# Kernel tuning notes

Hardware: AMD Instinct MI355X
Metric: run time of the kernel (lower is better)

The kernel has to match this reference:

```python
import jax, jax.numpy as jnp
import numpy as np

LATENT = 256


def setup_inputs() -> dict:
    key = jax.random.key(0)
    ks = jax.random.split(key, 10)
    B, T, V, E, D0, H, L = 512, 200, 3356, 1128, 20000, 1024, LATENT

    def glorot(k, shape):
        fan_out, fan_in = shape
        std = np.sqrt(2.0 / (fan_in + fan_out)).astype(np.float32)
        return jax.random.normal(k, shape, dtype=jnp.float32) * std

    x = jax.random.uniform(ks[0], (B, D0), dtype=jnp.float32)
    item_ids = jax.random.randint(ks[1], (B, T), 0, V, dtype=jnp.int32)
    embed = jax.random.normal(ks[2], (V, E), dtype=jnp.float32)
    Wi = glorot(ks[3], (L, E))
    bi = jnp.zeros((L,), jnp.float32)
    We1 = glorot(ks[4], (H, D0))
    be1 = jnp.zeros((H,), jnp.float32)
    We2 = glorot(ks[5], (2 * L, H))
    be2 = jnp.zeros((2 * L,), jnp.float32)
    Wd1 = glorot(ks[6], (H, L))
    bd1 = jnp.zeros((H,), jnp.float32)
    Wd2 = glorot(ks[7], (D0, H))
    bd2 = jnp.zeros((D0,), jnp.float32)
    # dropout(p=0.5) mask, pre-scaled by 1/(1-p)=2
    drop_mask = (jax.random.bernoulli(ks[8], 0.5, (B, D0))).astype(jnp.float32) * 2.0
    eps = jax.random.normal(ks[9], (B, L), dtype=jnp.float32)
    return {"x": x, "item_ids": item_ids, "embed": embed, "Wi": Wi, "bi": bi,
            "We1": We1, "be1": be1, "We2": We2, "be2": be2,
            "Wd1": Wd1, "bd1": bd1, "Wd2": Wd2, "bd2": bd2,
            "drop_mask": drop_mask, "eps": eps}


def reference(x, item_ids, embed, Wi, bi, We1, be1, We2, be2,
              Wd1, bd1, Wd2, bd2, drop_mask, eps):
    # item feature path: embedding lookup -> linear -> per-sequence stats
    item = jnp.einsum('bte,le->btl', embed[item_ids], Wi) + bi        # [B,T,L]
    mean = jnp.mean(item, axis=1)                                      # [B,L]
    deviation = jnp.std(item, axis=1, ddof=1)                          # torch.std (unbiased)

    # encoder: F.normalize (L2 over features) -> dropout -> tanh MLP
    xn = x / jnp.maximum(jnp.linalg.norm(x, axis=1, keepdims=True), 1e-12)
    h = xn * drop_mask
    h = jnp.tanh(h @ We1.T + be1)
    gparams = h @ We2.T + be2                                          # [B,2L]
    mu, logvar = gparams[:, :LATENT], gparams[:, LATENT:]

    # reparam: MVN with diagonal covariance diag(deviation) == mean + sqrt(dev)*eps
    prior = mean + jnp.sqrt(deviation) * eps
    z = prior * jnp.exp(0.5 * logvar) + mu

    # decoder: tanh MLP
    hd = jnp.tanh(z @ Wd1.T + bd1)
    recon_x = hd @ Wd2.T + bd2                                         # [B,D0]
    return recon_x, mu, logvar
```

## Files before the change

### kernel.cpp

```cpp
#include <hip/hip_runtime.h>
#include <hip/hip_bf16.h>

typedef __bf16 bf16x8 __attribute__((ext_vector_type(8)));
typedef float f32x4 __attribute__((ext_vector_type(4)));
typedef unsigned short u16x8 __attribute__((ext_vector_type(8)));

static __device__ __forceinline__ unsigned short f2bf(float f){
  unsigned int u = __float_as_uint(f);
  u += 0x7fffu + ((u >> 16) & 1u);
  return (unsigned short)(u >> 16);
}

static __device__ __forceinline__ u16x8 cvt8(const float4& a, const float4& b){
  u16x8 r;
  r[0]=f2bf(a.x); r[1]=f2bf(a.y); r[2]=f2bf(a.z); r[3]=f2bf(a.w);
  r[4]=f2bf(b.x); r[5]=f2bf(b.y); r[6]=f2bf(b.z); r[7]=f2bf(b.w);
  return r;
}

static __device__ __forceinline__ void gload16(const void* g, void* l){
  __builtin_amdgcn_global_load_lds(
      (const __attribute__((address_space(1))) unsigned int*)g,
      (__attribute__((address_space(3))) unsigned int*)l, 16, 0, 0);
}

static __device__ __forceinline__ int xcd_remap(int o, int nwg){
  const int NX = 8;
  int q = nwg / NX, r = nwg % NX;
  int xcd = o % NX, pos = o / NX;
  return (xcd < r ? xcd * (q + 1) : r * (q + 1) + (xcd - r) * q) + pos;
}

template<int EPI>
__global__ __launch_bounds__(256) void gemm_bf(
    const unsigned short* __restrict__ A, const unsigned short* __restrict__ Bw,
    const float* __restrict__ bias,
    float* __restrict__ Cf, unsigned short* __restrict__ Cbf,
    int M, int N, int K, int kchunk)
{
  constexpr int BM = 128, BN = 128, BK = 32, BUF = (BM + BN) * BK;
  __shared__ unsigned short lds[3 * BUF];

  const int gx = gridDim.x, gy = gridDim.y;
  const int nwg = gx * gy * gridDim.z;
  int o = blockIdx.x + gx * (blockIdx.y + gy * blockIdx.z);
  int v = xcd_remap(o, nwg);
  const int bx = v % gx; v /= gx;
  const int by = v % gy; const int bz = v / gy;

  const int tid  = threadIdx.x, lane = tid & 63, wave = tid >> 6;
  const int bm0  = by * BM, bn0 = bx * BN;
  const int k0   = bz * kchunk;
  const int kend = min(K, k0 + kchunk);
  const int fr = lane & 15, fq = lane >> 4;
  const int wm = (wave >> 1) * 64, wn = (wave & 1) * 64;

  const bool isA  = wave < 2;
  const int cbase = (wave & 1) * 4;
  const int srow  = lane >> 2, scol = (lane & 3) * 8;
  const unsigned short* G = isA ? A : Bw;
  const int glim = (isA ? M : N) - 1;
  const int g0   = isA ? bm0 : bn0;
  const int loff = isA ? 0 : BM * BK;

  const int nk = (kend - k0) / BK;

  auto stage = [&](int buf, int t){
    unsigned short* dst = lds + buf * BUF + loff;
    const int kk = k0 + t * BK;
    #pragma unroll
    for (int c = 0; c < 4; c++) {
      const int ch = cbase + c;
      const int r = min(g0 + ch * 16 + srow, glim);
      gload16(G + (size_t)r * K + kk + scol, (char*)dst + ch * 1024);
    }
  };

  if (nk > 0) stage(0, 0);
  if (nk > 1) stage(1, 1);
  if (nk > 2) stage(2, 2);

  f32x4 acc[4][4] = {};
  int cur = 0;

  for (int t = 0; t < nk; ++t) {
    const int rem = nk - t - 1;
    if (rem >= 2)      asm volatile("s_waitcnt vmcnt(8)" ::: "memory");
    else if (rem == 1) asm volatile("s_waitcnt vmcnt(4)" ::: "memory");
    else               asm volatile("s_waitcnt vmcnt(0)" ::: "memory");
    __builtin_amdgcn_s_barrier();
    __builtin_amdgcn_sched_barrier(0);

    const unsigned short* lA = lds + cur * BUF;
    const unsigned short* lB = lA + BM * BK;
    u16x8 af[4], bg[4];
    #pragma unroll
    for (int i = 0; i < 4; i++) af[i] = *(const u16x8*)&lA[(wm + i*16 + fr) * BK + fq * 8];
    #pragma unroll
    for (int j = 0; j < 4; j++) bg[j] = *(const u16x8*)&lB[(wn + j*16 + fr) * BK + fq * 8];

    #pragma unroll
    for (int i = 0; i < 4; i++)
      #pragma unroll
      for (int j = 0; j < 4; j++)
        acc[i][j] = __builtin_amdgcn_mfma_f32_16x16x32_bf16(
            __builtin_bit_cast(bf16x8, af[i]),
            __builtin_bit_cast(bf16x8, bg[j]),
            acc[i][j], 0, 0, 0);

    asm volatile("s_waitcnt lgkmcnt(0)" ::: "memory");
    __builtin_amdgcn_sched_barrier(0);
    __builtin_amdgcn_s_barrier();
    if (t + 3 < nk) stage(cur, t + 3);
    cur = (cur == 2) ? 0 : cur + 1;
  }

  #pragma unroll
  for (int i = 0; i < 4; i++)
    #pragma unroll
    for (int j = 0; j < 4; j++)
      #pragma unroll
      for (int r = 0; r < 4; r++) {
        int row = bm0 + wm + i*16 + fq*4 + r;
        int col = bn0 + wn + j*16 + fr;
        if (row < M && col < N) {
          float v2 = acc[i][j][r];
          if constexpr (EPI == 0) {
            Cf[(size_t)row * N + col] = v2 + (bias ? bias[col] : 0.0f);
          } else if constexpr (EPI == 1) {
            atomicAdd(&Cf[(size_t)row * N + col], v2);
          } else {
            Cbf[(size_t)row * N + col] = f2bf(tanhf(v2 + bias[col]));
          }
        }
      }
}

__global__ __launch_bounds__(256) void cvt4_kernel(
    const float* __restrict__ s0, unsigned short* __restrict__ d0, int n0,
    const float* __restrict__ s1, unsigned short* __restrict__ d1, int n1,
    const float* __restrict__ s2, unsigned short* __restrict__ d2, int n2,
    const float* __restrict__ s3, unsigned short* __restrict__ d3, int n3,
    int nunits16)
{
  const int stride = gridDim.x * 256;
  for (int u = blockIdx.x * 256 + threadIdx.x; u < nunits16; u += stride) {
    int i = u * 16;
    const float* s; unsigned short* d;
    if (i < n0)              { s = s0; d = d0; }
    else if ((i -= n0) < n1) { s = s1; d = d1; }
    else if ((i -= n1) < n2) { s = s2; d = d2; }
    else                     { i -= n2; s = s3; d = d3; }
    const float4* q = (const float4*)(s + i);
    float4 a0 = q[0], a1 = q[1], a2 = q[2], a3 = q[3];
    *(u16x8*)(d + i)     = cvt8(a0, a1);
    *(u16x8*)(d + i + 8) = cvt8(a2, a3);
  }
}

__global__ __launch_bounds__(256) void cvtpad_kernel(
    const float* __restrict__ src, unsigned short* __restrict__ dst,
    int rows, int scols, int dcols)
{
  int i8 = blockIdx.x * 256 + threadIdx.x;
  int c8 = dcols / 8;
  if (i8 >= rows * c8) return;
  int r = i8 / c8, c0 = (i8 % c8) * 8;
  const float* s = src + (size_t)r * scols;
  u16x8 o;
  #pragma unroll
  for (int e = 0; e < 8; e++) { int c = c0 + e; o[e] = (c < scols) ? f2bf(s[c]) : (unsigned short)0; }
  *(u16x8*)(dst + (size_t)r * dcols + c0) = o;
}

__global__ __launch_bounds__(256) void ynorm_kernel(
    const float* __restrict__ x, const float* __restrict__ dm,
    unsigned short* __restrict__ y, float* __restrict__ ninv, int D0)
{
  const int b = blockIdx.x, tid = threadIdx.x;
  const float4* x4 = (const float4*)(x + (size_t)b * D0);
  const float4* d4 = (const float4*)(dm + (size_t)b * D0);
  ushort4* y4 = (ushort4*)(y + (size_t)b * D0);
  const int n4 = D0 / 4;
  float ss = 0.f;
  for (int i = tid; i < n4; i += 256) {
    float4 xv = x4[i], dv = d4[i];
    ss += xv.x*xv.x + xv.y*xv.y + xv.z*xv.z + xv.w*xv.w;
    ushort4 o;
    o.x = f2bf(xv.x*dv.x); o.y = f2bf(xv.y*dv.y);
    o.z = f2bf(xv.z*dv.z); o.w = f2bf(xv.w*dv.w);
    y4[i] = o;
  }
  #pragma unroll
  for (int off = 32; off > 0; off >>= 1) ss += __shfl_down(ss, off);
  __shared__ float wsum[4];
  if ((tid & 63) == 0) wsum[tid >> 6] = ss;
  __syncthreads();
  if (tid == 0) {
    float t = wsum[0] + wsum[1] + wsum[2] + wsum[3];
    ninv[b] = 1.0f / fmaxf(sqrtf(t), 1e-12f);
  }
}

__global__ __launch_bounds__(256) void stats_kernel(
    const float* __restrict__ proj, const int* __restrict__ ids,
    const float* __restrict__ bi, const float* __restrict__ eps,
    float* __restrict__ prior, int T)
{
  const int b = blockIdx.x, l = threadIdx.x;
  __shared__ int sid[256];
  if (l < T) sid[l] = ids[b * T + l];
  __syncthreads();
  float s1 = 0.f, s2 = 0.f;
  #pragma unroll 4
  for (int t = 0; t < T; t++) {
    float p = proj[(size_t)sid[t] * 256 + l];
    s1 += p; s2 += p * p;
  }
  float var = fmaxf((s2 - s1 * s1 / (float)T) / (float)(T - 1), 0.f);
  float dev = sqrtf(var);
  float mean = s1 / (float)T + bi[l];
  prior[b * 256 + l] = mean + sqrtf(dev) * eps[b * 256 + l];
}

__global__ __launch_bounds__(256) void epi1_kernel(
    const float* __restrict__ C1, const float* __restrict__ ninv,
    const float* __restrict__ be1, unsigned short* __restrict__ h)
{
  int i = blockIdx.x * 256 + threadIdx.x;
  int b = i >> 10, n = i & 1023;
  h[i] = f2bf(tanhf(ninv[b] * C1[i] + be1[n]));
}

__global__ __launch_bounds__(256) void z_kernel(
    const float* __restrict__ gp, const float* __restrict__ prior,
    const float* __restrict__ be2,
    float* __restrict__ out_mu, float* __restrict__ out_lv,
    unsigned short* __restrict__ z)
{
  int i = blockIdx.x * 256 + threadIdx.x;
  int b = i >> 8, l = i & 255;
  float mu = gp[b * 512 + l]       + be2[l];
  float lv = gp[b * 512 + 256 + l] + be2[256 + l];
  out_mu[i] = mu;
  out_lv[i] = lv;
  z[i] = f2bf(prior[i] * expf(0.5f * lv) + mu);
}

extern "C" void kernel_launch(void* const* d_in, const int* in_sizes, int n_in,
                              void* d_out, int out_size, void* d_ws, size_t ws_size,
                              hipStream_t stream)
{
  const float* x     = (const float*)d_in[0];
  const int*   ids   = (const int*)  d_in[1];
  const float* embed = (const float*)d_in[2];
  const float* Wi    = (const float*)d_in[3];
  const float* bi    = (const float*)d_in[4];
  const float* We1   = (const float*)d_in[5];
  const float* be1   = (const float*)d_in[6];
  const float* We2   = (const float*)d_in[7];
  const float* be2   = (const float*)d_in[8];
  const float* Wd1   = (const float*)d_in[9];
  const float* bd1   = (const float*)d_in[10];
  const float* Wd2   = (const float*)d_in[11];
  const float* bd2   = (const float*)d_in[12];
  const float* dm    = (const float*)d_in[13];
  const float* eps   = (const float*)d_in[14];

  constexpr int B = 512, T = 200, V = 3356, E = 1128, Ep = 1152, D0 = 20000, H = 1024, L = 256;

  char* w = (char*)d_ws;
  auto carve = [&](size_t bytes) { char* p = w; w += (bytes + 255) & ~(size_t)255; return p; };
  unsigned short* We1b  = (unsigned short*)carve((size_t)H * D0 * 2);
  unsigned short* Wd2b  = (unsigned short*)carve((size_t)D0 * H * 2);
  unsigned short* We2b  = (unsigned short*)carve((size_t)2 * L * H * 2);
  unsigned short* Wd1b  = (unsigned short*)carve((size_t)H * L * 2);
  unsigned short* embedb= (unsigned short*)carve((size_t)V * Ep * 2);
  unsigned short* Wib   = (unsigned short*)carve((size_t)L * Ep * 2);
  float*          proj  = (float*)         carve((size_t)V * L * 4);
  unsigned short* y     = (unsigned short*)carve((size_t)B * D0 * 2);
  float*          C1    = (float*)         carve((size_t)B * H * 4);
  unsigned short* h     = (unsigned short*)carve((size_t)B * H * 2);
  float*          gp    = (float*)         carve((size_t)B * 2 * L * 4);
  float*          prior = (float*)         carve((size_t)B * L * 4);
  unsigned short* z     = (unsigned short*)carve((size_t)B * L * 2);
  unsigned short* hd    = (unsigned short*)carve((size_t)B * H * 2);
  float*          ninv  = (float*)         carve((size_t)B * 4);

  float* out_recon = (float*)d_out;
  float* out_mu    = out_recon + (size_t)B * D0;
  float* out_lv    = out_mu + (size_t)B * L;

  {
    const int n0 = H * D0, n1 = D0 * H, n2 = 2 * L * H, n3 = H * L;
    const int nunits16 = (n0 + n1 + n2 + n3) / 16;
    cvt4_kernel<<<2048, 256, 0, stream>>>(We1, We1b, n0, Wd2, Wd2b, n1,
                                          We2, We2b, n2, Wd1, Wd1b, n3, nunits16);
  }
  cvtpad_kernel<<<(V * (Ep/8) + 255) / 256, 256, 0, stream>>>(embed, embedb, V, E, Ep);
  cvtpad_kernel<<<(L * (Ep/8) + 255) / 256, 256, 0, stream>>>(Wi, Wib, L, E, Ep);

  ynorm_kernel<<<B, 256, 0, stream>>>(x, dm, y, ninv, D0);

  hipMemsetAsync(proj, 0, (size_t)V * L * 4, stream);
  gemm_bf<1><<<dim3(2, 27, 4), 256, 0, stream>>>(
      embedb, Wib, nullptr, proj, nullptr, V, L, Ep, 288);
  stats_kernel<<<B, 256, 0, stream>>>(proj, ids, bi, eps, prior, T);

  hipMemsetAsync(C1, 0, (size_t)B * H * 4, stream);
  gemm_bf<1><<<dim3(8, 4, 25), 256, 0, stream>>>(
      y, We1b, nullptr, C1, nullptr, B, H, D0, 800);
  epi1_kernel<<<(B * H) / 256, 256, 0, stream>>>(C1, ninv, be1, h);

  hipMemsetAsync(gp, 0, (size_t)B * 2 * L * 4, stream);
  gemm_bf<1><<<dim3(4, 4, 4), 256, 0, stream>>>(
      h, We2b, nullptr, gp, nullptr, B, 2 * L, H, 256);
  z_kernel<<<(B * L) / 256, 256, 0, stream>>>(gp, prior, be2, out_mu, out_lv, z);

  gemm_bf<2><<<dim3(8, 4, 1), 256, 0, stream>>>(
      z, Wd1b, bd1, nullptr, hd, B, H, L, 256);
  gemm_bf<0><<<dim3(157, 4, 1), 256, 0, stream>>>(
      hd, Wd2b, bd2, out_recon, nullptr, B, D0, H, 1024);
}
```

Baseline: 277.4 us.

## Single-barrier GEMM pipeline with prefetch distance two; merge prep kernels into one launch

The GEMM main loop drops its second barrier per K-step. The next stage load is now issued right after the top barrier into the buffer two ahead, so prefetch depth falls from three tiles to two. Separately, the weight conversion, embedding/Wi padding conversion and x-normalization kernels are merged into one block-indexed prep kernel to cut launch overhead and let those jobs run side by side. The shallower prefetch may expose more memory latency, and sizes are now hardcoded as constexpr in the prep kernel.

```diff
diff --git a/kernel.cpp b/kernel.cpp
--- a/kernel.cpp
+++ b/kernel.cpp
@@ -78,18 +78,20 @@
 
   if (nk > 0) stage(0, 0);
   if (nk > 1) stage(1, 1);
-  if (nk > 2) stage(2, 2);
 
   f32x4 acc[4][4] = {};
   int cur = 0;
 
   for (int t = 0; t < nk; ++t) {
-    const int rem = nk - t - 1;
-    if (rem >= 2)      asm volatile("s_waitcnt vmcnt(8)" ::: "memory");
-    else if (rem == 1) asm volatile("s_waitcnt vmcnt(4)" ::: "memory");
-    else               asm volatile("s_waitcnt vmcnt(0)" ::: "memory");
+    if (t < nk - 1) asm volatile("s_waitcnt vmcnt(4)" ::: "memory");
+    else            asm volatile("s_waitcnt vmcnt(0)" ::: "memory");
     __builtin_amdgcn_s_barrier();
     __builtin_amdgcn_sched_barrier(0);
+
+    if (t + 2 < nk) {
+      int sb = cur + 2; if (sb >= 3) sb -= 3;
+      stage(sb, t + 2);
+    }
 
     const unsigned short* lA = lds + cur * BUF;
     const unsigned short* lB = lA + BM * BK;
@@ -107,11 +109,6 @@
             __builtin_bit_cast(bf16x8, af[i]),
             __builtin_bit_cast(bf16x8, bg[j]),
             acc[i][j], 0, 0, 0);
-
-    asm volatile("s_waitcnt lgkmcnt(0)" ::: "memory");
-    __builtin_amdgcn_sched_barrier(0);
-    __builtin_amdgcn_s_barrier();
-    if (t + 3 < nk) stage(cur, t + 3);
     cur = (cur == 2) ? 0 : cur + 1;
   }
 
@@ -136,33 +133,10 @@
       }
 }
 
-__global__ __launch_bounds__(256) void cvt4_kernel(
-    const float* __restrict__ s0, unsigned short* __restrict__ d0, int n0,
-    const float* __restrict__ s1, unsigned short* __restrict__ d1, int n1,
-    const float* __restrict__ s2, unsigned short* __restrict__ d2, int n2,
-    const float* __restrict__ s3, unsigned short* __restrict__ d3, int n3,
-    int nunits16)
-{
-  const int stride = gridDim.x * 256;
-  for (int u = blockIdx.x * 256 + threadIdx.x; u < nunits16; u += stride) {
-    int i = u * 16;
-    const float* s; unsigned short* d;
-    if (i < n0)              { s = s0; d = d0; }
-    else if ((i -= n0) < n1) { s = s1; d = d1; }
-    else if ((i -= n1) < n2) { s = s2; d = d2; }
-    else                     { i -= n2; s = s3; d = d3; }
-    const float4* q = (const float4*)(s + i);
-    float4 a0 = q[0], a1 = q[1], a2 = q[2], a3 = q[3];
-    *(u16x8*)(d + i)     = cvt8(a0, a1);
-    *(u16x8*)(d + i + 8) = cvt8(a2, a3);
-  }
-}
-
-__global__ __launch_bounds__(256) void cvtpad_kernel(
+static __device__ __forceinline__ void cvtpad_body(
     const float* __restrict__ src, unsigned short* __restrict__ dst,
-    int rows, int scols, int dcols)
-{
-  int i8 = blockIdx.x * 256 + threadIdx.x;
+    int rows, int scols, int dcols, int i8)
+{
   int c8 = dcols / 8;
   if (i8 >= rows * c8) return;
   int r = i8 / c8, c0 = (i8 % c8) * 8;
@@ -173,32 +147,65 @@
   *(u16x8*)(dst + (size_t)r * dcols + c0) = o;
 }
 
-__global__ __launch_bounds__(256) void ynorm_kernel(
+__global__ __launch_bounds__(256) void prep_kernel(
+    const float* __restrict__ We1, unsigned short* __restrict__ We1b,
+    const float* __restrict__ Wd2, unsigned short* __restrict__ Wd2b,
+    const float* __restrict__ We2, unsigned short* __restrict__ We2b,
+    const float* __restrict__ Wd1, unsigned short* __restrict__ Wd1b,
+    const float* __restrict__ embed, unsigned short* __restrict__ embedb,
+    const float* __restrict__ Wi, unsigned short* __restrict__ Wib,
     const float* __restrict__ x, const float* __restrict__ dm,
-    unsigned short* __restrict__ y, float* __restrict__ ninv, int D0)
-{
-  const int b = blockIdx.x, tid = threadIdx.x;
-  const float4* x4 = (const float4*)(x + (size_t)b * D0);
-  const float4* d4 = (const float4*)(dm + (size_t)b * D0);
-  ushort4* y4 = (ushort4*)(y + (size_t)b * D0);
-  const int n4 = D0 / 4;
-  float ss = 0.f;
-  for (int i = tid; i < n4; i += 256) {
-    float4 xv = x4[i], dv = d4[i];
-    ss += xv.x*xv.x + xv.y*xv.y + xv.z*xv.z + xv.w*xv.w;
-    ushort4 o;
-    o.x = f2bf(xv.x*dv.x); o.y = f2bf(xv.y*dv.y);
-    o.z = f2bf(xv.z*dv.z); o.w = f2bf(xv.w*dv.w);
-    y4[i] = o;
-  }
-  #pragma unroll
-  for (int off = 32; off > 0; off >>= 1) ss += __shfl_down(ss, off);
-  __shared__ float wsum[4];
-  if ((tid & 63) == 0) wsum[tid >> 6] = ss;
-  __syncthreads();
-  if (tid == 0) {
-    float t = wsum[0] + wsum[1] + wsum[2] + wsum[3];
-    ninv[b] = 1.0f / fmaxf(sqrtf(t), 1e-12f);
+    unsigned short* __restrict__ y, float* __restrict__ ninv)
+{
+  constexpr int D0 = 20000, H = 1024, L = 256, V = 3356, E = 1128, Ep = 1152;
+  constexpr int n0 = H * D0, n1 = D0 * H, n2 = 2 * L * H, n3 = H * L;
+  constexpr int CVT_B = 2048, YN_B = 512;
+  constexpr int PE_B = (V * (Ep / 8) + 255) / 256;
+  const int bb = blockIdx.x, tid = threadIdx.x;
+
+  if (bb < CVT_B) {
+    constexpr int nunits16 = (n0 + n1 + n2 + n3) / 16;
+    const int stride = CVT_B * 256;
+    for (int u = bb * 256 + tid; u < nunits16; u += stride) {
+      int i = u * 16;
+      const float* s; unsigned short* d;
+      if (i < n0)              { s = We1; d = We1b; }
+      else if ((i -= n0) < n1) { s = Wd2; d = Wd2b; }
+      else if ((i -= n1) < n2) { s = We2; d = We2b; }
+      else                     { i -= n2; s = Wd1; d = Wd1b; }
+      const float4* q = (const float4*)(s + i);
+      float4 a0 = q[0], a1 = q[1], a2 = q[2], a3 = q[3];
+      *(u16x8*)(d + i)     = cvt8(a0, a1);
+      *(u16x8*)(d + i + 8) = cvt8(a2, a3);
+    }
+  } else if (bb < CVT_B + YN_B) {
+    const int b = bb - CVT_B;
+    const float4* x4 = (const float4*)(x + (size_t)b * D0);
+    const float4* d4 = (const float4*)(dm + (size_t)b * D0);
+    ushort4* y4 = (ushort4*)(y + (size_t)b * D0);
+    const int n4 = D0 / 4;
+    float ss = 0.f;
+    for (int i = tid; i < n4; i += 256) {
+      float4 xv = x4[i], dv = d4[i];
+      ss += xv.x*xv.x + xv.y*xv.y + xv.z*xv.z + xv.w*xv.w;
+      ushort4 ov;
+      ov.x = f2bf(xv.x*dv.x); ov.y = f2bf(xv.y*dv.y);
+      ov.z = f2bf(xv.z*dv.z); ov.w = f2bf(xv.w*dv.w);
+      y4[i] = ov;
+    }
+    #pragma unroll
+    for (int off = 32; off > 0; off >>= 1) ss += __shfl_down(ss, off);
+    __shared__ float wsum[4];
+    if ((tid & 63) == 0) wsum[tid >> 6] = ss;
+    __syncthreads();
+    if (tid == 0) {
+      float t = wsum[0] + wsum[1] + wsum[2] + wsum[3];
+      ninv[b] = 1.0f / fmaxf(sqrtf(t), 1e-12f);
+    }
+  } else if (bb < CVT_B + YN_B + PE_B) {
+    cvtpad_body(embed, embedb, V, E, Ep, (bb - (CVT_B + YN_B)) * 256 + tid);
+  } else {
+    cvtpad_body(Wi, Wib, L, E, Ep, (bb - (CVT_B + YN_B + PE_B)) * 256 + tid);
   }
 }
 
@@ -292,15 +299,13 @@
   float* out_lv    = out_mu + (size_t)B * L;
 
   {
-    const int n0 = H * D0, n1 = D0 * H, n2 = 2 * L * H, n3 = H * L;
-    const int nunits16 = (n0 + n1 + n2 + n3) / 16;
-    cvt4_kernel<<<2048, 256, 0, stream>>>(We1, We1b, n0, Wd2, Wd2b, n1,
-                                          We2, We2b, n2, Wd1, Wd1b, n3, nunits16);
+    constexpr int CVT_B = 2048, YN_B = 512;
+    constexpr int PE_B = (V * (Ep / 8) + 255) / 256;
+    constexpr int PW_B = (L * (Ep / 8) + 255) / 256;
+    prep_kernel<<<CVT_B + YN_B + PE_B + PW_B, 256, 0, stream>>>(
+        We1, We1b, Wd2, Wd2b, We2, We2b, Wd1, Wd1b,
+        embed, embedb, Wi, Wib, x, dm, y, ninv);
   }
-  cvtpad_kernel<<<(V * (Ep/8) + 255) / 256, 256, 0, stream>>>(embed, embedb, V, E, Ep);
-  cvtpad_kernel<<<(L * (Ep/8) + 255) / 256, 256, 0, stream>>>(Wi, Wib, L, E, Ep);
-
-  ynorm_kernel<<<B, 256, 0, stream>>>(x, dm, y, ninv, D0);
 
   hipMemsetAsync(proj, 0, (size_t)V * L * 4, stream);
   gemm_bf<1><<<dim3(2, 27, 4), 256, 0, stream>>>(
```

Result: faster. 259.9 us (median of 2 runs) (-6.3%).
